# Performance work log

Hardware: AMD Instinct MI355X
Metric: run time of the kernel (lower is better)

The kernel has to match this reference:

```python
import jax, jax.numpy as jnp
import numpy as np

B, N, D, P = 16, 128, 1024, 128  # batch, seq_len, n_in, n_mlp
SCALE = 0  # scores divided by P**SCALE (supar convention); scale=0 => no-op


def setup_inputs() -> dict:
    key = jax.random.key(0)
    ks = jax.random.split(key, 6)
    s_in = 1.0 / np.sqrt(D)   # keep MLP activations ~unit scale
    s_w = 1.0 / P             # keep triple-product scores bounded
    return {
        "x": jax.random.normal(ks[0], (B, N, D), jnp.float32),
        "x_span": jax.random.normal(ks[1], (B, N, D), jnp.float32),
        # MLP projections (Linear weight stored torch-style as (out, in))
        "Wx": jax.random.normal(ks[2], (P, D), jnp.float32) * s_in,
        "bx": jnp.zeros((P,), jnp.float32),
        "Wy": jax.random.normal(ks[3], (P, D), jnp.float32) * s_in,
        "by": jnp.zeros((P,), jnp.float32),
        "Wz": jax.random.normal(ks[4], (P, D), jnp.float32) * s_in,
        "bz": jnp.zeros((P,), jnp.float32),
        # Triaffine weight: (P+1 [bias_x], P [z, no bias], P+1 [bias_y]), n_out=1 squeezed
        "W3": jax.random.normal(ks[5], (P + 1, P, P + 1), jnp.float32) * s_w,
    }


def _mlp(h, W, b):
    # supar MLP: Linear + LeakyReLU(0.1); dropout=0 at inference
    return jax.nn.leaky_relu(h @ W.T + b, 0.1)


def reference(x, x_span, Wx, bx, Wy, by, Wz, bz, W3):
    xp = _mlp(x_span, Wx, bx)  # (B,N,P)  -> triaffine arg x
    yp = _mlp(x_span, Wy, by)  # (B,N,P)  -> triaffine arg y
    zp = _mlp(x, Wz, bz)       # (B,N,P)  -> triaffine arg z (head words)
    ones = jnp.ones((B, N, 1), xp.dtype)
    x1 = jnp.concatenate([xp, ones], axis=-1)  # bias_x
    y1 = jnp.concatenate([yp, ones], axis=-1)  # bias_y
    # w: per-head-word bilinear map, (B,N,P+1,P+1)
    w = jnp.einsum('bzk,ikj->bzij', zp, W3)
    # s: (B, z, x, y) = (B,N,N,N)
    s = jnp.einsum('bxi,bzij,byj->bzxy', x1, w, y1)
    s = s / (P ** SCALE)
    # Span2oScorer: s.permute(0, 2, 3, 1).float() -> (B, span_i, span_j, head)
    return jnp.transpose(s, (0, 2, 3, 1)).astype(jnp.float32)
```

## Files before the change

kernel.cpp:

```cpp
#include <hip/hip_runtime.h>

typedef __bf16 bf16;
typedef __bf16 bf16x8 __attribute__((ext_vector_type(8)));
typedef __bf16 bf16x4 __attribute__((ext_vector_type(4)));
typedef float f32x4 __attribute__((ext_vector_type(4)));

#define MFMA(a, b, c) __builtin_amdgcn_mfma_f32_16x16x32_bf16((a), (b), (c), 0, 0, 0)

static __device__ __forceinline__ f32x4 zero4() {
    f32x4 z; z[0] = 0.f; z[1] = 0.f; z[2] = 0.f; z[3] = 0.f; return z;
}

static __device__ __forceinline__ void soft_barrier() {
    __builtin_amdgcn_sched_barrier(0);
    asm volatile("s_waitcnt lgkmcnt(0)" ::: "memory");
    __builtin_amdgcn_s_barrier();
    __builtin_amdgcn_sched_barrier(0);
}

__global__ __launch_bounds__(256) void k_prep(
    const float* __restrict__ Wx, const float* __restrict__ Wy, const float* __restrict__ Wz,
    const float* __restrict__ W3,
    bf16* __restrict__ wbf, bf16* __restrict__ w3b, float* __restrict__ w3bias)
{
    const int b = blockIdx.x, t = threadIdx.x;
    if (b < 96) {
        int proj = b >> 5;
        const float* src = (proj == 0) ? Wx : (proj == 1) ? Wy : Wz;
        bf16* dst = wbf + proj * 131072;
        int o = (b & 31) * 4096 + t * 16;
#pragma unroll
        for (int u = 0; u < 4; u++) {
            float4 v = *(const float4*)(src + o + u * 4);
            bf16x4 w; w[0] = (bf16)v.x; w[1] = (bf16)v.y; w[2] = (bf16)v.z; w[3] = (bf16)v.w;
            *(bf16x4*)(dst + o + u * 4) = w;
        }
    } else {
        int nb = b - 96;
        int n = nb * 8 + (t >> 5);
        int c = t & 31;
        const float* row = W3 + n * 129;
        float v0 = row[4 * c + 0];
        float v1 = row[4 * c + 1];
        float v2 = row[4 * c + 2];
        float v3 = row[4 * c + 3];
        bf16x4 w;
        w[0] = (bf16)v0; w[1] = (bf16)v1; w[2] = (bf16)v2; w[3] = (bf16)v3;
        *(bf16x4*)(w3b + n * 136 + 4 * c) = w;
        if (c == 0) w3bias[n] = row[128];
    }
}

__global__ __launch_bounds__(256) void k_mlp(
    const float* __restrict__ xsp, const float* __restrict__ x,
    const bf16* __restrict__ wbf,
    const float* __restrict__ bx, const float* __restrict__ by, const float* __restrict__ bz,
    bf16* __restrict__ pout)
{
    __shared__ bf16 Al[16 * 1032];
    const int proj = blockIdx.y;
    const float* A = (proj == 2) ? x : xsp;
    const bf16* W = wbf + proj * 131072;
    const float* bias = (proj == 0) ? bx : (proj == 1) ? by : bz;
    bf16* out = pout + proj * 262144;

    const int tid = threadIdx.x;
    const int wv = tid >> 6, lane = tid & 63, quad = lane >> 4, lr = lane & 15;
    const int m0 = blockIdx.x * 16;

    {
        const float* Asrc = A + m0 * 1024;
        const int rr = tid >> 7, cc = (tid & 127) * 8;
#pragma unroll
        for (int i = 0; i < 8; i++) {
            int r = i * 2 + rr;
            float4 v0 = *(const float4*)(Asrc + r * 1024 + cc);
            float4 v1 = *(const float4*)(Asrc + r * 1024 + cc + 4);
            bf16x8 w;
            w[0] = (bf16)v0.x; w[1] = (bf16)v0.y; w[2] = (bf16)v0.z; w[3] = (bf16)v0.w;
            w[4] = (bf16)v1.x; w[5] = (bf16)v1.y; w[6] = (bf16)v1.z; w[7] = (bf16)v1.w;
            *(bf16x8*)(&Al[r * 1032 + cc]) = w;
        }
    }
    __syncthreads();

    f32x4 acc[2];
    acc[0] = zero4(); acc[1] = zero4();

    const bf16* brow = Al + lr * 1032 + quad * 8;
    const bf16* arow = W + (wv * 16 + lr) * 1024 + quad * 8;

#pragma unroll 4
    for (int kw = 0; kw < 32; kw++) {
        bf16x8 bfr = *(const bf16x8*)(brow + kw * 32);
        bf16x8 a0 = *(const bf16x8*)(arow + kw * 32);
        bf16x8 a1 = *(const bf16x8*)(arow + 65536 + kw * 32);
        acc[0] = MFMA(a0, bfr, acc[0]);
        acc[1] = MFMA(a1, bfr, acc[1]);
    }
#pragma unroll
    for (int s = 0; s < 2; s++) {
        int p = (wv + s * 4) * 16 + quad * 4;
        float4 bv = *(const float4*)(bias + p);
        int m = m0 + lr;
        bf16x4 o;
        float v0 = acc[s][0] + bv.x; o[0] = (bf16)(v0 > 0.f ? v0 : 0.1f * v0);
        float v1 = acc[s][1] + bv.y; o[1] = (bf16)(v1 > 0.f ? v1 : 0.1f * v1);
        float v2 = acc[s][2] + bv.z; o[2] = (bf16)(v2 > 0.f ? v2 : 0.1f * v2);
        float v3 = acc[s][3] + bv.w; o[3] = (bf16)(v3 > 0.f ? v3 : 0.1f * v3);
        *(bf16x4*)(out + m * 128 + p) = o;
    }
}

__global__ __launch_bounds__(256, 4) void k_vgemm(
    const bf16* __restrict__ yp,
    const bf16* __restrict__ w3b,
    const float* __restrict__ w3bias,
    bf16* __restrict__ V)
{
    __shared__ bf16 Vt[128 * 136];
    const int b = blockIdx.x;
    const int n0 = blockIdx.y * 128;
    const int tid = threadIdx.x;
    const int wv = tid >> 6, lane = tid & 63, quad = lane >> 4, lr = lane & 15;
    const int y0 = wv * 32;

    const bf16* Ab = yp + b * 16384;

    f32x4 acc[8][2];
#pragma unroll
    for (int nt = 0; nt < 8; nt++) { acc[nt][0] = zero4(); acc[nt][1] = zero4(); }

#pragma unroll
    for (int kw = 0; kw < 4; kw++) {
        bf16x8 b0 = *(const bf16x8*)(Ab + (y0 + lr) * 128 + kw * 32 + quad * 8);
        bf16x8 b1 = *(const bf16x8*)(Ab + (y0 + 16 + lr) * 128 + kw * 32 + quad * 8);
#pragma unroll
        for (int nt = 0; nt < 8; nt++) {
            bf16x8 af = *(const bf16x8*)(w3b + (n0 + nt * 16 + lr) * 136 + kw * 32 + quad * 8);
            acc[nt][0] = MFMA(af, b0, acc[nt][0]);
            acc[nt][1] = MFMA(af, b1, acc[nt][1]);
        }
    }
#pragma unroll
    for (int nt = 0; nt < 8; nt++) {
        int nl = nt * 16 + quad * 4;
        float4 bv = *(const float4*)(w3bias + n0 + nl);
#pragma unroll
        for (int s = 0; s < 2; s++) {
            int y = y0 + s * 16 + lr;
            bf16x4 o;
            o[0] = (bf16)(acc[nt][s][0] + bv.x);
            o[1] = (bf16)(acc[nt][s][1] + bv.y);
            o[2] = (bf16)(acc[nt][s][2] + bv.z);
            o[3] = (bf16)(acc[nt][s][3] + bv.w);
            *(bf16x4*)(&Vt[y * 136 + nl]) = o;
        }
    }
    __syncthreads();
    const int yr = tid >> 4, nn = (tid & 15) * 8;
#pragma unroll
    for (int pass = 0; pass < 8; pass++) {
        int y = pass * 16 + yr;
        bf16x8 v = *(const bf16x8*)(&Vt[y * 136 + nn]);
        *(bf16x8*)(V + (b * 128 + y) * 16512 + n0 + nn) = v;
    }
}

__global__ __launch_bounds__(256, 2) void k_score(
    const bf16* __restrict__ xp,
    const bf16* __restrict__ zp,
    const bf16* __restrict__ V,
    float* __restrict__ out)
{
    __shared__ __align__(16) bf16 Vl[2][129 * 136];
    __shared__ float Hb[128];
    const int tid = threadIdx.x;
    const int wv = tid >> 6, lane = tid & 63, quad = lane >> 4, lr = lane & 15;
    const int c0 = wv * 32;

    const int it0 = blockIdx.x * 4;
    const int b = it0 >> 7;
    const int y0 = it0 & 127;

    const bf16* Zb = zp + b * 16384;
    const bf16* Xb = xp + b * 16384;
    const bf16* Vbase = V + (b * 128 + y0) * 16512;

    bf16x8 st[8], st4;
#pragma unroll
    for (int q = 0; q < 8; q++) st4[q] = (bf16)0.f;
#pragma unroll
    for (int u = 0; u < 8; u++) st[u] = *(const bf16x8*)(Vbase + (tid + u * 256) * 8);
    if (tid < 16) st4 = *(const bf16x8*)(Vbase + (2048 + tid) * 8);

    bf16x8 bz[4][2], bxf[4][2];
#pragma unroll
    for (int kw = 0; kw < 4; kw++)
#pragma unroll
        for (int s = 0; s < 2; s++)
            bz[kw][s] = *(const bf16x8*)(Zb + (c0 + s * 16 + lr) * 128 + kw * 32 + quad * 8);
#pragma unroll
    for (int iw = 0; iw < 4; iw++)
#pragma unroll
        for (int s = 0; s < 2; s++)
            bxf[iw][s] = *(const bf16x8*)(Xb + (c0 + s * 16 + lr) * 128 + iw * 32 + quad * 8);

#pragma unroll 1
    for (int n = 0; n < 4; n++) {
        bf16* Bc = &Vl[n & 1][0];

#pragma unroll
        for (int u = 0; u < 8; u++) {
            int c = tid + u * 256;
            *(bf16x8*)(Bc + (c >> 4) * 136 + (c & 15) * 8) = st[u];
        }
        if (tid < 16) *(bf16x8*)(Bc + 128 * 136 + tid * 8) = st4;
        soft_barrier();

        f32x4 acc1[9][2];
#pragma unroll
        for (int it = 0; it < 9; it++) { acc1[it][0] = zero4(); acc1[it][1] = zero4(); }

#pragma unroll
        for (int kw = 0; kw < 4; kw++) {
#pragma unroll
            for (int it = 0; it < 8; it++) {
                bf16x8 af = *(const bf16x8*)(Bc + (it * 16 + lr) * 136 + kw * 32 + quad * 8);
                acc1[it][0] = MFMA(af, bz[kw][0], acc1[it][0]);
                acc1[it][1] = MFMA(af, bz[kw][1], acc1[it][1]);
            }
            bf16x8 a8;
#pragma unroll
            for (int q = 0; q < 8; q++) a8[q] = (bf16)0.f;
            if (lr == 0) a8 = *(const bf16x8*)(Bc + 128 * 136 + kw * 32 + quad * 8);
            acc1[8][0] = MFMA(a8, bz[kw][0], acc1[8][0]);
            acc1[8][1] = MFMA(a8, bz[kw][1], acc1[8][1]);
        }
        soft_barrier();

#pragma unroll
        for (int it = 0; it < 8; it++) {
            int i = it * 16 + quad * 4;
#pragma unroll
            for (int s = 0; s < 2; s++) {
                bf16x4 o;
                o[0] = (bf16)acc1[it][s][0];
                o[1] = (bf16)acc1[it][s][1];
                o[2] = (bf16)acc1[it][s][2];
                o[3] = (bf16)acc1[it][s][3];
                *(bf16x4*)(Bc + (c0 + s * 16 + lr) * 136 + i) = o;
            }
        }
        if (quad == 0) {
            Hb[c0 + lr]      = acc1[8][0][0];
            Hb[c0 + 16 + lr] = acc1[8][1][0];
        }
        soft_barrier();

        if (n < 3) {
            const bf16* Vnx = Vbase + (n + 1) * 16512;
#pragma unroll
            for (int u = 0; u < 8; u++) st[u] = *(const bf16x8*)(Vnx + (tid + u * 256) * 8);
            if (tid < 16) st4 = *(const bf16x8*)(Vnx + (2048 + tid) * 8);
        }

        f32x4 acc2[8][2];
#pragma unroll
        for (int zt = 0; zt < 8; zt++) { acc2[zt][0] = zero4(); acc2[zt][1] = zero4(); }

#pragma unroll
        for (int iw = 0; iw < 4; iw++) {
#pragma unroll
            for (int zt = 0; zt < 8; zt++) {
                bf16x8 ah = *(const bf16x8*)(Bc + (zt * 16 + lr) * 136 + iw * 32 + quad * 8);
                acc2[zt][0] = MFMA(ah, bxf[iw][0], acc2[zt][0]);
                acc2[zt][1] = MFMA(ah, bxf[iw][1], acc2[zt][1]);
            }
        }
#pragma unroll
        for (int zt = 0; zt < 8; zt++) {
            int zb = zt * 16 + quad * 4;
            f32x4 hb = *(const f32x4*)(&Hb[zb]);
#pragma unroll
            for (int s = 0; s < 2; s++) {
                int xx = c0 + s * 16 + lr;
                f32x4 o;
                o[0] = acc2[zt][s][0] + hb[0];
                o[1] = acc2[zt][s][1] + hb[1];
                o[2] = acc2[zt][s][2] + hb[2];
                o[3] = acc2[zt][s][3] + hb[3];
                *(f32x4*)(out + (((b * 128 + xx) * 128 + (y0 + n)) * 128 + zb)) = o;
            }
        }
    }
}

extern "C" void kernel_launch(void* const* d_in, const int* in_sizes, int n_in,
                              void* d_out, int out_size, void* d_ws, size_t ws_size,
                              hipStream_t stream) {
    const float* x   = (const float*)d_in[0];
    const float* xsp = (const float*)d_in[1];
    const float* Wx  = (const float*)d_in[2];
    const float* bx  = (const float*)d_in[3];
    const float* Wy  = (const float*)d_in[4];
    const float* by  = (const float*)d_in[5];
    const float* Wz  = (const float*)d_in[6];
    const float* bz  = (const float*)d_in[7];
    const float* W3  = (const float*)d_in[8];
    float* out = (float*)d_out;

    char* ws = (char*)d_ws;
    bf16*  wbf    = (bf16*)(ws + 8388608);
    bf16*  w3b    = (bf16*)(ws + 9175040);
    bf16*  pout   = (bf16*)(ws + 13666304);
    bf16*  V      = (bf16*)(ws + 15239168);
    float* w3bias = (float*)(ws + 82872320);

    k_prep<<<2160, 256, 0, stream>>>(Wx, Wy, Wz, W3, wbf, w3b, w3bias);
    k_mlp<<<dim3(128, 3), 256, 0, stream>>>(xsp, x, wbf, bx, by, bz, pout);
    k_vgemm<<<dim3(16, 129), 256, 0, stream>>>(pout + 262144 , w3b, w3bias, V);
    k_score<<<512, 256, 0, stream>>>(pout , pout + 524288 , V, out);
}
```

Before: 241.3 us.

## Retile score kernel warps into 2x2 64x64 tiles and reload operands per step

Each wave now computes a 64x64 output tile (split across rows and columns) in place of a 128x32 strip in both GEMM stages, so LDS A-fragment reads are halved per MFMA. The Z and X B-fragments are loaded from global memory inside each iteration, not held in registers across the loop, which cuts register pressure but adds repeated global/L2 loads. Wave priority is raised around the MFMA loops via s_setprio, and the bias row MFMA is done only by half the waves.

After: 277.3 us. +14.9%, slower.

```diff
diff --git a/kernel.cpp b/kernel.cpp
--- a/kernel.cpp
+++ b/kernel.cpp
@@ -177,7 +177,8 @@
     __shared__ float Hb[128];
     const int tid = threadIdx.x;
     const int wv = tid >> 6, lane = tid & 63, quad = lane >> 4, lr = lane & 15;
-    const int c0 = wv * 32;
+    const int ih = wv & 1;
+    const int ch = wv >> 1;
 
     const int it0 = blockIdx.x * 4;
     const int b = it0 >> 7;
@@ -194,18 +195,6 @@
     for (int u = 0; u < 8; u++) st[u] = *(const bf16x8*)(Vbase + (tid + u * 256) * 8);
     if (tid < 16) st4 = *(const bf16x8*)(Vbase + (2048 + tid) * 8);
 
-    bf16x8 bz[4][2], bxf[4][2];
-#pragma unroll
-    for (int kw = 0; kw < 4; kw++)
-#pragma unroll
-        for (int s = 0; s < 2; s++)
-            bz[kw][s] = *(const bf16x8*)(Zb + (c0 + s * 16 + lr) * 128 + kw * 32 + quad * 8);
-#pragma unroll
-    for (int iw = 0; iw < 4; iw++)
-#pragma unroll
-        for (int s = 0; s < 2; s++)
-            bxf[iw][s] = *(const bf16x8*)(Xb + (c0 + s * 16 + lr) * 128 + iw * 32 + quad * 8);
-
 #pragma unroll 1
     for (int n = 0; n < 4; n++) {
         bf16* Bc = &Vl[n & 1][0];
@@ -216,45 +205,65 @@
             *(bf16x8*)(Bc + (c >> 4) * 136 + (c & 15) * 8) = st[u];
         }
         if (tid < 16) *(bf16x8*)(Bc + 128 * 136 + tid * 8) = st4;
+
+        bf16x8 bz[4][4];
+#pragma unroll
+        for (int kw = 0; kw < 4; kw++)
+#pragma unroll
+            for (int s = 0; s < 4; s++)
+                bz[kw][s] = *(const bf16x8*)(Zb + (ch * 64 + s * 16 + lr) * 128 + kw * 32 + quad * 8);
+
         soft_barrier();
 
-        f32x4 acc1[9][2];
-#pragma unroll
-        for (int it = 0; it < 9; it++) { acc1[it][0] = zero4(); acc1[it][1] = zero4(); }
-
+        f32x4 acc1[5][4];
+#pragma unroll
+        for (int it = 0; it < 5; it++)
+#pragma unroll
+            for (int s = 0; s < 4; s++) acc1[it][s] = zero4();
+
+        __builtin_amdgcn_s_setprio(1);
 #pragma unroll
         for (int kw = 0; kw < 4; kw++) {
 #pragma unroll
-            for (int it = 0; it < 8; it++) {
-                bf16x8 af = *(const bf16x8*)(Bc + (it * 16 + lr) * 136 + kw * 32 + quad * 8);
-                acc1[it][0] = MFMA(af, bz[kw][0], acc1[it][0]);
-                acc1[it][1] = MFMA(af, bz[kw][1], acc1[it][1]);
-            }
-            bf16x8 a8;
-#pragma unroll
-            for (int q = 0; q < 8; q++) a8[q] = (bf16)0.f;
-            if (lr == 0) a8 = *(const bf16x8*)(Bc + 128 * 136 + kw * 32 + quad * 8);
-            acc1[8][0] = MFMA(a8, bz[kw][0], acc1[8][0]);
-            acc1[8][1] = MFMA(a8, bz[kw][1], acc1[8][1]);
-        }
+            for (int it = 0; it < 4; it++) {
+                bf16x8 af = *(const bf16x8*)(Bc + (ih * 64 + it * 16 + lr) * 136 + kw * 32 + quad * 8);
+#pragma unroll
+                for (int s = 0; s < 4; s++) acc1[it][s] = MFMA(af, bz[kw][s], acc1[it][s]);
+            }
+            if (ih == 0) {
+                bf16x8 a8;
+#pragma unroll
+                for (int q = 0; q < 8; q++) a8[q] = (bf16)0.f;
+                if (lr == 0) a8 = *(const bf16x8*)(Bc + 128 * 136 + kw * 32 + quad * 8);
+#pragma unroll
+                for (int s = 0; s < 4; s++) acc1[4][s] = MFMA(a8, bz[kw][s], acc1[4][s]);
+            }
+        }
+        __builtin_amdgcn_s_setprio(0);
         soft_barrier();
 
-#pragma unroll
-        for (int it = 0; it < 8; it++) {
-            int i = it * 16 + quad * 4;
-#pragma unroll
-            for (int s = 0; s < 2; s++) {
+        bf16x8 bxf[4][4];
+#pragma unroll
+        for (int iw = 0; iw < 4; iw++)
+#pragma unroll
+            for (int s = 0; s < 4; s++)
+                bxf[iw][s] = *(const bf16x8*)(Xb + (ch * 64 + s * 16 + lr) * 128 + iw * 32 + quad * 8);
+
+#pragma unroll
+        for (int it = 0; it < 4; it++) {
+#pragma unroll
+            for (int s = 0; s < 4; s++) {
                 bf16x4 o;
                 o[0] = (bf16)acc1[it][s][0];
                 o[1] = (bf16)acc1[it][s][1];
                 o[2] = (bf16)acc1[it][s][2];
                 o[3] = (bf16)acc1[it][s][3];
-                *(bf16x4*)(Bc + (c0 + s * 16 + lr) * 136 + i) = o;
-            }
-        }
-        if (quad == 0) {
-            Hb[c0 + lr]      = acc1[8][0][0];
-            Hb[c0 + 16 + lr] = acc1[8][1][0];
+                *(bf16x4*)(Bc + (ch * 64 + s * 16 + lr) * 136 + ih * 64 + it * 16 + quad * 4) = o;
+            }
+        }
+        if (ih == 0 && quad == 0) {
+#pragma unroll
+            for (int s = 0; s < 4; s++) Hb[ch * 64 + s * 16 + lr] = acc1[4][s][0];
         }
         soft_barrier();
 
@@ -265,26 +274,31 @@
             if (tid < 16) st4 = *(const bf16x8*)(Vnx + (2048 + tid) * 8);
         }
 
-        f32x4 acc2[8][2];
-#pragma unroll
-        for (int zt = 0; zt < 8; zt++) { acc2[zt][0] = zero4(); acc2[zt][1] = zero4(); }
-
+        f32x4 acc2[4][4];
+#pragma unroll
+        for (int zt = 0; zt < 4; zt++)
+#pragma unroll
+            for (int s = 0; s < 4; s++) acc2[zt][s] = zero4();
+
+        __builtin_amdgcn_s_setprio(1);
 #pragma unroll
         for (int iw = 0; iw < 4; iw++) {
 #pragma unroll
-            for (int zt = 0; zt < 8; zt++) {
-                bf16x8 ah = *(const bf16x8*)(Bc + (zt * 16 + lr) * 136 + iw * 32 + quad * 8);
-                acc2[zt][0] = MFMA(ah, bxf[iw][0], acc2[zt][0]);
-                acc2[zt][1] = MFMA(ah, bxf[iw][1], acc2[zt][1]);
-            }
-        }
-#pragma unroll
-        for (int zt = 0; zt < 8; zt++) {
-            int zb = zt * 16 + quad * 4;
+            for (int zt = 0; zt < 4; zt++) {
+                bf16x8 ah = *(const bf16x8*)(Bc + (ih * 64 + zt * 16 + lr) * 136 + iw * 32 + quad * 8);
+#pragma unroll
+                for (int s = 0; s < 4; s++) acc2[zt][s] = MFMA(ah, bxf[iw][s], acc2[zt][s]);
+            }
+        }
+        __builtin_amdgcn_s_setprio(0);
+
+#pragma unroll
+        for (int zt = 0; zt < 4; zt++) {
+            int zb = ih * 64 + zt * 16 + quad * 4;
             f32x4 hb = *(const f32x4*)(&Hb[zb]);
 #pragma unroll
-            for (int s = 0; s < 2; s++) {
-                int xx = c0 + s * 16 + lr;
+            for (int s = 0; s < 4; s++) {
+                int xx = ch * 64 + s * 16 + lr;
                 f32x4 o;
                 o[0] = acc2[zt][s][0] + hb[0];
                 o[1] = acc2[zt][s][1] + hb[1];
```
